# Optimization experiments

Measured on AMD Instinct MI355X. Metric: run time of the kernel, lower is better.

The kernel has to match this reference:

```python
import jax, jax.numpy as jnp
import numpy as np

NB = 16   # num_blocks
DIN = 64  # per-block input dim
DOUT = 64 # per-block output dim
NT = 2    # n_templates (ns)


def setup_inputs() -> dict:
    key = jax.random.key(0)
    k1, k2, k3, k4, k5 = jax.random.split(key, 5)
    T, B = 2048, 8
    a = 0.1  # GroupLinearLayer init range
    x = jax.random.normal(k1, (T, B, NB * DIN), dtype=jnp.float32)
    module_emb = 0.1 * jax.random.normal(k2, (1, 1, NB * DIN), dtype=jnp.float32)
    read_w = jax.random.uniform(k3, (1, DIN, NT), dtype=jnp.float32, minval=-a, maxval=a)
    lim = 1.0 / np.sqrt(DIN)  # nn.Linear default init range
    w_stack = jax.random.uniform(k4, (NT, DOUT, DIN), dtype=jnp.float32, minval=-lim, maxval=lim)
    b_stack = jax.random.uniform(k5, (NT, DOUT), dtype=jnp.float32, minval=-lim, maxval=lim)
    return {"x": x, "module_emb": module_emb, "read_w": read_w,
            "w_stack": w_stack, "b_stack": b_stack}


def reference(x, module_emb, read_w, w_stack, b_stack):
    T, B, D = x.shape
    # add module embedding (broadcast over T, B)
    new_x = x + module_emb
    # flatten to per-block tokens: (N, DIN) with N = T*B*NB
    xf = new_x.reshape(T * B * NB, DIN)
    # routing logits via GroupLinearLayer with 1 block: (N, NT)
    logits = xf @ read_w[0]
    att = jax.nn.softmax(logits, axis=-1)
    # apply each template Linear: (N, NT, DOUT)
    x_next = jnp.einsum('nd,tod->nto', xf, w_stack) + b_stack[None, :, :]
    # soft combine templates; mean over singleton dim is identity
    out = jnp.einsum('nt,nto->no', att, x_next)
    return out.reshape(T, B, NB * DOUT)
```

## Files before the change

### kernel.cpp

```cpp
#include <hip/hip_runtime.h>


#define NBLK 1024

typedef short bf16x8 __attribute__((ext_vector_type(8)));
typedef float f32x4  __attribute__((ext_vector_type(4)));

union B8 { bf16x8 v; unsigned u[4]; };

__device__ __forceinline__ unsigned pk2bf(float lo, float hi) {
    unsigned a = __float_as_uint(lo) + 0x8000u;
    unsigned b = __float_as_uint(hi) + 0x8000u;
    return __builtin_amdgcn_perm(b, a, 0x07060302u);
}

__device__ __forceinline__ void pack8(B8& d, float4 p, float4 q) {
    d.u[0] = pk2bf(p.x, p.y); d.u[1] = pk2bf(p.z, p.w);
    d.u[2] = pk2bf(q.x, q.y); d.u[3] = pk2bf(q.z, q.w);
}

__global__ __launch_bounds__(256, 4) void sgll_kernel(
    const float* __restrict__ x,
    const float* __restrict__ emb,
    const float* __restrict__ rw,
    const float* __restrict__ ws,
    const float* __restrict__ bs,
    float* __restrict__ out)
{
    __shared__ bf16x8 sW1[8][64];
    __shared__ bf16x8 sWd[8][64];
    __shared__ f32x4  sI1[4][64];
    __shared__ f32x4  sId[4][64];
    __shared__ f32x4  sIl[64];

    const int tid  = threadIdx.x;
    const int lane = tid & 63;
    const int wv   = tid >> 6;
    const int col  = lane & 15;
    const int q    = lane >> 4;

    #pragma unroll
    for (int c = wv; c < 8; c += 4) {
        const int kt = c >> 2, ot = c & 3;
        const float* p0 = ws + (ot * 16 + col) * 64 + kt * 32 + q * 8;
        const float* p1 = p0 + 4096;
        float4 a0 = *(const float4*)p0, a1 = *(const float4*)(p0 + 4);
        float4 c0 = *(const float4*)p1, c1 = *(const float4*)(p1 + 4);
        B8 f1, fd;
        pack8(f1, make_float4(c0.x, c0.y, c0.z, c0.w), c1);
        fd.u[0] = pk2bf(a0.x - c0.x, a0.y - c0.y);
        fd.u[1] = pk2bf(a0.z - c0.z, a0.w - c0.w);
        fd.u[2] = pk2bf(a1.x - c1.x, a1.y - c1.y);
        fd.u[3] = pk2bf(a1.z - c1.z, a1.w - c1.w);
        sW1[c][lane] = f1.v;
        sWd[c][lane] = fd.v;
    }

    B8 R0, R1;
    {
        float v[8];
        #pragma unroll
        for (int j = 0; j < 8; ++j)
            v[j] = (col < 2) ? rw[(q * 8 + j) * 2 + col] : 0.f;
        pack8(R0, make_float4(v[0], v[1], v[2], v[3]), make_float4(v[4], v[5], v[6], v[7]));
        #pragma unroll
        for (int j = 0; j < 8; ++j)
            v[j] = (col < 2) ? rw[(32 + q * 8 + j) * 2 + col] : 0.f;
        pack8(R1, make_float4(v[0], v[1], v[2], v[3]), make_float4(v[4], v[5], v[6], v[7]));
    }

    __syncthreads();

    if (wv == 0) {
        const float* ep = emb + col * 64 + q * 8;
        float4 e0 = *(const float4*)ep,        e1 = *(const float4*)(ep + 4);
        float4 e2 = *(const float4*)(ep + 32), e3 = *(const float4*)(ep + 36);
        B8 E0, E1;
        pack8(E0, e0, e1);
        pack8(E1, e2, e3);
        #pragma unroll
        for (int ot = 0; ot < 4; ++ot) {
            float4 b1 = *(const float4*)(bs + 64 + ot * 16 + q * 4);
            float4 b0 = *(const float4*)(bs + ot * 16 + q * 4);
            f32x4 a1 = {b1.x, b1.y, b1.z, b1.w};
            f32x4 ad = {b0.x - b1.x, b0.y - b1.y, b0.z - b1.z, b0.w - b1.w};
            a1 = __builtin_amdgcn_mfma_f32_16x16x32_bf16(sW1[ot][lane],     E0.v, a1, 0, 0, 0);
            a1 = __builtin_amdgcn_mfma_f32_16x16x32_bf16(sW1[4 + ot][lane], E1.v, a1, 0, 0, 0);
            ad = __builtin_amdgcn_mfma_f32_16x16x32_bf16(sWd[ot][lane],     E0.v, ad, 0, 0, 0);
            ad = __builtin_amdgcn_mfma_f32_16x16x32_bf16(sWd[4 + ot][lane], E1.v, ad, 0, 0, 0);
            sI1[ot][lane] = a1;
            sId[ot][lane] = ad;
        }
        f32x4 zl = {0.f, 0.f, 0.f, 0.f};
        zl = __builtin_amdgcn_mfma_f32_16x16x32_bf16(R0.v, E0.v, zl, 0, 0, 0);
        zl = __builtin_amdgcn_mfma_f32_16x16x32_bf16(R1.v, E1.v, zl, 0, 0, 0);
        sIl[lane] = zl;
    }
    __syncthreads();

    const long base = (long)(blockIdx.x * 4 + wv) * 64;
    float4 A[3][4];

    #define LOAD_TILE(buf, t)  do {                                        \
        const float* p = x + (base + (long)(t) * 16 + col) * 64 + q * 8;   \
        A[buf][0] = *(const float4*)p;        A[buf][1] = *(const float4*)(p + 4);  \
        A[buf][2] = *(const float4*)(p + 32); A[buf][3] = *(const float4*)(p + 36); \
    } while (0)

    LOAD_TILE(0, 0);
    LOAD_TILE(1, 1);

    #pragma unroll
    for (int i = 0; i < 4; ++i) {
        const int b = i % 3;
        if (i + 2 < 4) LOAD_TILE((i + 2) % 3, i + 2);

        B8 X0, X1;
        pack8(X0, A[b][0], A[b][1]);
        pack8(X1, A[b][2], A[b][3]);

        f32x4 lac = sIl[lane];
        lac = __builtin_amdgcn_mfma_f32_16x16x32_bf16(R0.v, X0.v, lac, 0, 0, 0);
        lac = __builtin_amdgcn_mfma_f32_16x16x32_bf16(R1.v, X1.v, lac, 0, 0, 0);
        float att = 1.0f / (1.0f + __expf(lac[1] - lac[0]));
        att = __shfl(att, col);

        const long rowoff = (base + (long)i * 16 + col) * 64;
        #pragma unroll
        for (int ot = 0; ot < 4; ++ot) {
            f32x4 y = sI1[ot][lane];
            y = __builtin_amdgcn_mfma_f32_16x16x32_bf16(sW1[ot][lane],     X0.v, y, 0, 0, 0);
            y = __builtin_amdgcn_mfma_f32_16x16x32_bf16(sW1[4 + ot][lane], X1.v, y, 0, 0, 0);
            f32x4 d = sId[ot][lane];
            d = __builtin_amdgcn_mfma_f32_16x16x32_bf16(sWd[ot][lane],     X0.v, d, 0, 0, 0);
            d = __builtin_amdgcn_mfma_f32_16x16x32_bf16(sWd[4 + ot][lane], X1.v, d, 0, 0, 0);
            float4 o;
            o.x = fmaf(att, d[0], y[0]);
            o.y = fmaf(att, d[1], y[1]);
            o.z = fmaf(att, d[2], y[2]);
            o.w = fmaf(att, d[3], y[3]);
            *(float4*)(out + rowoff + ot * 16 + q * 4) = o;
        }
    }
    #undef LOAD_TILE
}

extern "C" void kernel_launch(void* const* d_in, const int* in_sizes, int n_in,
                              void* d_out, int out_size, void* d_ws, size_t ws_size,
                              hipStream_t stream) {
    const float* x   = (const float*)d_in[0];
    const float* emb = (const float*)d_in[1];
    const float* rw  = (const float*)d_in[2];
    const float* wsk = (const float*)d_in[3];
    const float* bs  = (const float*)d_in[4];
    float* out = (float*)d_out;
    sgll_kernel<<<NBLK, 256, 0, stream>>>(x, emb, rw, wsk, bs, out);
}
```

Measured before the change: 132.0 us.

## Issue all x tile loads upfront and compute embedding/bias terms per wave in registers

Every wave now computes the embedding-plus-bias intercepts in registers, replacing the single wave that computed them and shared them through LDS. This removes one __syncthreads and the LDS round trip for those values. All four x tiles are loaded at once before the intercept MFMAs, with a sched_barrier so the loads go out first and the intercept work hides their latency. Register pressure rises, so launch bounds drop to 3 blocks per SM, trading occupancy for more memory-level parallelism.

```diff
diff --git a/kernel.cpp b/kernel.cpp
--- a/kernel.cpp
+++ b/kernel.cpp
@@ -19,7 +19,7 @@
     d.u[2] = pk2bf(q.x, q.y); d.u[3] = pk2bf(q.z, q.w);
 }
 
-__global__ __launch_bounds__(256, 4) void sgll_kernel(
+__global__ __launch_bounds__(256, 3) void sgll_kernel(
     const float* __restrict__ x,
     const float* __restrict__ emb,
     const float* __restrict__ rw,
@@ -29,9 +29,6 @@
 {
     __shared__ bf16x8 sW1[8][64];
     __shared__ bf16x8 sWd[8][64];
-    __shared__ f32x4  sI1[4][64];
-    __shared__ f32x4  sId[4][64];
-    __shared__ f32x4  sIl[64];
 
     const int tid  = threadIdx.x;
     const int lane = tid & 63;
@@ -47,7 +44,7 @@
         float4 a0 = *(const float4*)p0, a1 = *(const float4*)(p0 + 4);
         float4 c0 = *(const float4*)p1, c1 = *(const float4*)(p1 + 4);
         B8 f1, fd;
-        pack8(f1, make_float4(c0.x, c0.y, c0.z, c0.w), c1);
+        pack8(f1, c0, c1);
         fd.u[0] = pk2bf(a0.x - c0.x, a0.y - c0.y);
         fd.u[1] = pk2bf(a0.z - c0.z, a0.w - c0.w);
         fd.u[2] = pk2bf(a1.x - c1.x, a1.y - c1.y);
@@ -69,57 +66,59 @@
         pack8(R1, make_float4(v[0], v[1], v[2], v[3]), make_float4(v[4], v[5], v[6], v[7]));
     }
 
-    __syncthreads();
+    B8 E0, E1;
+    {
+        const float* ep = emb + col * 64 + q * 8;
+        pack8(E0, *(const float4*)ep, *(const float4*)(ep + 4));
+        pack8(E1, *(const float4*)(ep + 32), *(const float4*)(ep + 36));
+    }
+    f32x4 bI1[4], bId[4];
+    #pragma unroll
+    for (int ot = 0; ot < 4; ++ot) {
+        float4 b1 = *(const float4*)(bs + 64 + ot * 16 + q * 4);
+        float4 b0 = *(const float4*)(bs + ot * 16 + q * 4);
+        bI1[ot][0] = b1.x; bI1[ot][1] = b1.y; bI1[ot][2] = b1.z; bI1[ot][3] = b1.w;
+        bId[ot][0] = b0.x - b1.x; bId[ot][1] = b0.y - b1.y;
+        bId[ot][2] = b0.z - b1.z; bId[ot][3] = b0.w - b1.w;
+    }
 
-    if (wv == 0) {
-        const float* ep = emb + col * 64 + q * 8;
-        float4 e0 = *(const float4*)ep,        e1 = *(const float4*)(ep + 4);
-        float4 e2 = *(const float4*)(ep + 32), e3 = *(const float4*)(ep + 36);
-        B8 E0, E1;
-        pack8(E0, e0, e1);
-        pack8(E1, e2, e3);
-        #pragma unroll
-        for (int ot = 0; ot < 4; ++ot) {
-            float4 b1 = *(const float4*)(bs + 64 + ot * 16 + q * 4);
-            float4 b0 = *(const float4*)(bs + ot * 16 + q * 4);
-            f32x4 a1 = {b1.x, b1.y, b1.z, b1.w};
-            f32x4 ad = {b0.x - b1.x, b0.y - b1.y, b0.z - b1.z, b0.w - b1.w};
-            a1 = __builtin_amdgcn_mfma_f32_16x16x32_bf16(sW1[ot][lane],     E0.v, a1, 0, 0, 0);
-            a1 = __builtin_amdgcn_mfma_f32_16x16x32_bf16(sW1[4 + ot][lane], E1.v, a1, 0, 0, 0);
-            ad = __builtin_amdgcn_mfma_f32_16x16x32_bf16(sWd[ot][lane],     E0.v, ad, 0, 0, 0);
-            ad = __builtin_amdgcn_mfma_f32_16x16x32_bf16(sWd[4 + ot][lane], E1.v, ad, 0, 0, 0);
-            sI1[ot][lane] = a1;
-            sId[ot][lane] = ad;
-        }
-        f32x4 zl = {0.f, 0.f, 0.f, 0.f};
-        zl = __builtin_amdgcn_mfma_f32_16x16x32_bf16(R0.v, E0.v, zl, 0, 0, 0);
-        zl = __builtin_amdgcn_mfma_f32_16x16x32_bf16(R1.v, E1.v, zl, 0, 0, 0);
-        sIl[lane] = zl;
-    }
     __syncthreads();
 
     const long base = (long)(blockIdx.x * 4 + wv) * 64;
-    float4 A[3][4];
+    float4 buf[4][4];
+    #pragma unroll
+    for (int t = 0; t < 4; ++t) {
+        const float* p = x + (base + (long)t * 16 + col) * 64 + q * 8;
+        buf[t][0] = *(const float4*)p;        buf[t][1] = *(const float4*)(p + 4);
+        buf[t][2] = *(const float4*)(p + 32); buf[t][3] = *(const float4*)(p + 36);
+    }
+    __builtin_amdgcn_sched_barrier(0);
 
-    #define LOAD_TILE(buf, t)  do {                                        \
-        const float* p = x + (base + (long)(t) * 16 + col) * 64 + q * 8;   \
-        A[buf][0] = *(const float4*)p;        A[buf][1] = *(const float4*)(p + 4);  \
-        A[buf][2] = *(const float4*)(p + 32); A[buf][3] = *(const float4*)(p + 36); \
-    } while (0)
-
-    LOAD_TILE(0, 0);
-    LOAD_TILE(1, 1);
+    f32x4 I1[4], Id[4], Il;
+    #pragma unroll
+    for (int ot = 0; ot < 4; ++ot) {
+        f32x4 a1 = bI1[ot], ad = bId[ot];
+        a1 = __builtin_amdgcn_mfma_f32_16x16x32_bf16(sW1[ot][lane],     E0.v, a1, 0, 0, 0);
+        a1 = __builtin_amdgcn_mfma_f32_16x16x32_bf16(sW1[4 + ot][lane], E1.v, a1, 0, 0, 0);
+        ad = __builtin_amdgcn_mfma_f32_16x16x32_bf16(sWd[ot][lane],     E0.v, ad, 0, 0, 0);
+        ad = __builtin_amdgcn_mfma_f32_16x16x32_bf16(sWd[4 + ot][lane], E1.v, ad, 0, 0, 0);
+        I1[ot] = a1;
+        Id[ot] = ad;
+    }
+    {
+        f32x4 z = {0.f, 0.f, 0.f, 0.f};
+        z = __builtin_amdgcn_mfma_f32_16x16x32_bf16(R0.v, E0.v, z, 0, 0, 0);
+        z = __builtin_amdgcn_mfma_f32_16x16x32_bf16(R1.v, E1.v, z, 0, 0, 0);
+        Il = z;
+    }
 
     #pragma unroll
     for (int i = 0; i < 4; ++i) {
-        const int b = i % 3;
-        if (i + 2 < 4) LOAD_TILE((i + 2) % 3, i + 2);
+        B8 X0, X1;
+        pack8(X0, buf[i][0], buf[i][1]);
+        pack8(X1, buf[i][2], buf[i][3]);
 
-        B8 X0, X1;
-        pack8(X0, A[b][0], A[b][1]);
-        pack8(X1, A[b][2], A[b][3]);
-
-        f32x4 lac = sIl[lane];
+        f32x4 lac = Il;
         lac = __builtin_amdgcn_mfma_f32_16x16x32_bf16(R0.v, X0.v, lac, 0, 0, 0);
         lac = __builtin_amdgcn_mfma_f32_16x16x32_bf16(R1.v, X1.v, lac, 0, 0, 0);
         float att = 1.0f / (1.0f + __expf(lac[1] - lac[0]));
@@ -128,10 +127,10 @@
         const long rowoff = (base + (long)i * 16 + col) * 64;
         #pragma unroll
         for (int ot = 0; ot < 4; ++ot) {
-            f32x4 y = sI1[ot][lane];
+            f32x4 y = I1[ot];
             y = __builtin_amdgcn_mfma_f32_16x16x32_bf16(sW1[ot][lane],     X0.v, y, 0, 0, 0);
             y = __builtin_amdgcn_mfma_f32_16x16x32_bf16(sW1[4 + ot][lane], X1.v, y, 0, 0, 0);
-            f32x4 d = sId[ot][lane];
+            f32x4 d = Id[ot];
             d = __builtin_amdgcn_mfma_f32_16x16x32_bf16(sWd[ot][lane],     X0.v, d, 0, 0, 0);
             d = __builtin_amdgcn_mfma_f32_16x16x32_bf16(sWd[4 + ot][lane], X1.v, d, 0, 0, 0);
             float4 o;
@@ -142,7 +141,6 @@
             *(float4*)(out + rowoff + ot * 16 + q * 4) = o;
         }
     }
-    #undef LOAD_TILE
 }
 
 extern "C" void kernel_launch(void* const* d_in, const int* in_sizes, int n_in,
```

New measurement: 128.6 us. 2.6% less time.

## Use 512-thread blocks with two tiles per wave and shared routing weights

Applied to the files above, without the earlier changes.

Doubles the block to 512 threads (8 waves) so each wave handles 32 rows instead of 64, and loads both of its tiles up front rather than through a triple-buffered prefetch. The routing-weight fragments move from per-thread registers into shared memory. Each wave now packs exactly one weight chunk during setup. The aim is more resident waves per CU to hide memory latency, at the cost of a higher per-row share of block setup and extra LDS reads inside the loop.

```diff
diff --git a/kernel.cpp b/kernel.cpp
--- a/kernel.cpp
+++ b/kernel.cpp
@@ -19,7 +19,7 @@
     d.u[2] = pk2bf(q.x, q.y); d.u[3] = pk2bf(q.z, q.w);
 }
 
-__global__ __launch_bounds__(256, 4) void sgll_kernel(
+__global__ __launch_bounds__(512, 8) void sgll_kernel(
     const float* __restrict__ x,
     const float* __restrict__ emb,
     const float* __restrict__ rw,
@@ -29,6 +29,7 @@
 {
     __shared__ bf16x8 sW1[8][64];
     __shared__ bf16x8 sWd[8][64];
+    __shared__ bf16x8 sR0[64], sR1[64];
     __shared__ f32x4  sI1[4][64];
     __shared__ f32x4  sId[4][64];
     __shared__ f32x4  sIl[64];
@@ -39,45 +40,44 @@
     const int col  = lane & 15;
     const int q    = lane >> 4;
 
-    #pragma unroll
-    for (int c = wv; c < 8; c += 4) {
-        const int kt = c >> 2, ot = c & 3;
+    {
+        const int kt = wv >> 2, ot = wv & 3;
         const float* p0 = ws + (ot * 16 + col) * 64 + kt * 32 + q * 8;
         const float* p1 = p0 + 4096;
         float4 a0 = *(const float4*)p0, a1 = *(const float4*)(p0 + 4);
         float4 c0 = *(const float4*)p1, c1 = *(const float4*)(p1 + 4);
         B8 f1, fd;
-        pack8(f1, make_float4(c0.x, c0.y, c0.z, c0.w), c1);
+        pack8(f1, c0, c1);
         fd.u[0] = pk2bf(a0.x - c0.x, a0.y - c0.y);
         fd.u[1] = pk2bf(a0.z - c0.z, a0.w - c0.w);
         fd.u[2] = pk2bf(a1.x - c1.x, a1.y - c1.y);
         fd.u[3] = pk2bf(a1.z - c1.z, a1.w - c1.w);
-        sW1[c][lane] = f1.v;
-        sWd[c][lane] = fd.v;
+        sW1[wv][lane] = f1.v;
+        sWd[wv][lane] = fd.v;
     }
 
-    B8 R0, R1;
-    {
+    if (wv == 1) {
         float v[8];
+        B8 r;
         #pragma unroll
         for (int j = 0; j < 8; ++j)
             v[j] = (col < 2) ? rw[(q * 8 + j) * 2 + col] : 0.f;
-        pack8(R0, make_float4(v[0], v[1], v[2], v[3]), make_float4(v[4], v[5], v[6], v[7]));
+        pack8(r, make_float4(v[0], v[1], v[2], v[3]), make_float4(v[4], v[5], v[6], v[7]));
+        sR0[lane] = r.v;
         #pragma unroll
         for (int j = 0; j < 8; ++j)
             v[j] = (col < 2) ? rw[(32 + q * 8 + j) * 2 + col] : 0.f;
-        pack8(R1, make_float4(v[0], v[1], v[2], v[3]), make_float4(v[4], v[5], v[6], v[7]));
+        pack8(r, make_float4(v[0], v[1], v[2], v[3]), make_float4(v[4], v[5], v[6], v[7]));
+        sR1[lane] = r.v;
     }
 
     __syncthreads();
 
     if (wv == 0) {
+        B8 E0, E1;
         const float* ep = emb + col * 64 + q * 8;
-        float4 e0 = *(const float4*)ep,        e1 = *(const float4*)(ep + 4);
-        float4 e2 = *(const float4*)(ep + 32), e3 = *(const float4*)(ep + 36);
-        B8 E0, E1;
-        pack8(E0, e0, e1);
-        pack8(E1, e2, e3);
+        pack8(E0, *(const float4*)ep, *(const float4*)(ep + 4));
+        pack8(E1, *(const float4*)(ep + 32), *(const float4*)(ep + 36));
         #pragma unroll
         for (int ot = 0; ot < 4; ++ot) {
             float4 b1 = *(const float4*)(bs + 64 + ot * 16 + q * 4);
@@ -91,37 +91,32 @@
             sI1[ot][lane] = a1;
             sId[ot][lane] = ad;
         }
-        f32x4 zl = {0.f, 0.f, 0.f, 0.f};
-        zl = __builtin_amdgcn_mfma_f32_16x16x32_bf16(R0.v, E0.v, zl, 0, 0, 0);
-        zl = __builtin_amdgcn_mfma_f32_16x16x32_bf16(R1.v, E1.v, zl, 0, 0, 0);
-        sIl[lane] = zl;
+        f32x4 z = {0.f, 0.f, 0.f, 0.f};
+        z = __builtin_amdgcn_mfma_f32_16x16x32_bf16(sR0[lane], E0.v, z, 0, 0, 0);
+        z = __builtin_amdgcn_mfma_f32_16x16x32_bf16(sR1[lane], E1.v, z, 0, 0, 0);
+        sIl[lane] = z;
     }
     __syncthreads();
 
-    const long base = (long)(blockIdx.x * 4 + wv) * 64;
-    float4 A[3][4];
-
-    #define LOAD_TILE(buf, t)  do {                                        \
-        const float* p = x + (base + (long)(t) * 16 + col) * 64 + q * 8;   \
-        A[buf][0] = *(const float4*)p;        A[buf][1] = *(const float4*)(p + 4);  \
-        A[buf][2] = *(const float4*)(p + 32); A[buf][3] = *(const float4*)(p + 36); \
-    } while (0)
-
-    LOAD_TILE(0, 0);
-    LOAD_TILE(1, 1);
+    const long base = (long)(blockIdx.x * 8 + wv) * 32;
+    float4 buf[2][4];
+    #pragma unroll
+    for (int t = 0; t < 2; ++t) {
+        const float* p = x + (base + (long)t * 16 + col) * 64 + q * 8;
+        buf[t][0] = *(const float4*)p;        buf[t][1] = *(const float4*)(p + 4);
+        buf[t][2] = *(const float4*)(p + 32); buf[t][3] = *(const float4*)(p + 36);
+    }
+    __builtin_amdgcn_sched_barrier(0);
 
     #pragma unroll
-    for (int i = 0; i < 4; ++i) {
-        const int b = i % 3;
-        if (i + 2 < 4) LOAD_TILE((i + 2) % 3, i + 2);
-
+    for (int i = 0; i < 2; ++i) {
         B8 X0, X1;
-        pack8(X0, A[b][0], A[b][1]);
-        pack8(X1, A[b][2], A[b][3]);
+        pack8(X0, buf[i][0], buf[i][1]);
+        pack8(X1, buf[i][2], buf[i][3]);
 
         f32x4 lac = sIl[lane];
-        lac = __builtin_amdgcn_mfma_f32_16x16x32_bf16(R0.v, X0.v, lac, 0, 0, 0);
-        lac = __builtin_amdgcn_mfma_f32_16x16x32_bf16(R1.v, X1.v, lac, 0, 0, 0);
+        lac = __builtin_amdgcn_mfma_f32_16x16x32_bf16(sR0[lane], X0.v, lac, 0, 0, 0);
+        lac = __builtin_amdgcn_mfma_f32_16x16x32_bf16(sR1[lane], X1.v, lac, 0, 0, 0);
         float att = 1.0f / (1.0f + __expf(lac[1] - lac[0]));
         att = __shfl(att, col);
 
@@ -142,7 +137,6 @@
             *(float4*)(out + rowoff + ot * 16 + q * 4) = o;
         }
     }
-    #undef LOAD_TILE
 }
 
 extern "C" void kernel_launch(void* const* d_in, const int* in_sizes, int n_in,
@@ -154,5 +148,5 @@
     const float* wsk = (const float*)d_in[3];
     const float* bs  = (const float*)d_in[4];
     float* out = (float*)d_out;
-    sgll_kernel<<<NBLK, 256, 0, stream>>>(x, emb, rw, wsk, bs, out);
+    sgll_kernel<<<NBLK, 512, 0, stream>>>(x, emb, rw, wsk, bs, out);
 }
```

Measured after the change: 131.0 us. About the same (-0.8%).
